# Kernel optimization log

Hardware: AMD Instinct MI355X
Metric: run time of the kernel (lower is better)

Reference implementation:

```python
import jax, jax.numpy as jnp
import numpy as np


def setup_inputs() -> dict:
    key = jax.random.key(0)
    ks = jax.random.split(key, 6)
    SEQ, B, N_INP, N_HID, N_OUT = 2048, 128, 64, 128, 10
    # orthogonal-ish init scales (rand_ortho produces orthogonal matrices; we use
    # scaled gaussians as stand-ins since exact values don't affect the op pattern)
    x = jax.random.normal(ks[0], (SEQ, B, N_INP), dtype=jnp.float32)
    Wxh = jax.random.normal(ks[1], (N_INP, N_HID), dtype=jnp.float32) * np.sqrt(1.0 / N_INP).astype(np.float32)
    Whh = jax.random.normal(ks[2], (N_HID, N_HID), dtype=jnp.float32) * np.sqrt(1.0 / N_HID).astype(np.float32)
    Why = jax.random.normal(ks[3], (N_HID, N_OUT), dtype=jnp.float32) * np.sqrt(1.0 / N_HID).astype(np.float32)
    bh = jnp.zeros((N_HID,), dtype=jnp.float32)
    by = jnp.zeros((N_OUT,), dtype=jnp.float32)
    return {"x": x, "Wxh": Wxh, "Whh": Whh, "Why": Why, "bh": bh, "by": by}


def reference(x, Wxh, Whh, Why, bh, by):
    # x: [seq_len, batch, n_inp]
    seq_len, batch, _ = x.shape
    n_hid = Whh.shape[0]
    # precompute the input projection for all timesteps in one big GEMM
    xW = jnp.einsum('sbi,ih->sbh', x, Wxh) + bh  # [S, B, H]

    def step(h_prev, xw_t):
        h_t = jnp.tanh(h_prev @ Whh + xw_t)
        return h_t, h_t

    h0 = jnp.zeros((batch, n_hid), dtype=x.dtype)
    h_last, h = jax.lax.scan(step, h0, xW)  # h: [S, B, H]
    logits = h_last @ Why + by  # [B, n_out]
    return (logits, h)
```

## Files before the change

### kernel.cpp

```cpp
#include <hip/hip_runtime.h>
#include <math.h>

#define SEQ   2048
#define BATCH  128
#define NINP    64
#define NHID   128
#define NOUT    10
#define CH      64
#define NCHUNK (SEQ / CH)

typedef const float __attribute__((address_space(1)))* gptr_t;
typedef float       __attribute__((address_space(3)))* lptr_t;

__global__ __launch_bounds__(256) void proj_kernel(const float* __restrict__ x,
                                                   const float* __restrict__ Wxh,
                                                   const float* __restrict__ bh,
                                                   float* __restrict__ xw) {
    __shared__ float Wlds[NINP * NHID];
    __shared__ float xs[32 * NINP];
    const int t = threadIdx.x;
    const size_t r0 = (size_t)blockIdx.x * 32;

#pragma unroll
    for (int i = 0; i < 8; ++i)
        ((float4*)Wlds)[t + 256 * i] = ((const float4*)Wxh)[t + 256 * i];
    const float4* xg = (const float4*)(x + r0 * NINP);
    ((float4*)xs)[t]       = xg[t];
    ((float4*)xs)[t + 256] = xg[t + 256];
    __syncthreads();

    const int tj = t & 31;
    const int tr = t >> 5;
    const int j  = 4 * tj;
    const float4 bhv = *(const float4*)(bh + j);
    float acc[4][4];
#pragma unroll
    for (int r = 0; r < 4; ++r) {
        acc[r][0] = bhv.x; acc[r][1] = bhv.y; acc[r][2] = bhv.z; acc[r][3] = bhv.w;
    }
#pragma unroll 8
    for (int i = 0; i < NINP; ++i) {
        const float4 w4 = *(const float4*)&Wlds[i * NHID + j];
#pragma unroll
        for (int r = 0; r < 4; ++r) {
            const float xv = xs[(4 * tr + r) * NINP + i];
            acc[r][0] = fmaf(xv, w4.x, acc[r][0]);
            acc[r][1] = fmaf(xv, w4.y, acc[r][1]);
            acc[r][2] = fmaf(xv, w4.z, acc[r][2]);
            acc[r][3] = fmaf(xv, w4.w, acc[r][3]);
        }
    }
#pragma unroll
    for (int r = 0; r < 4; ++r) {
        float4 o = { acc[r][0], acc[r][1], acc[r][2], acc[r][3] };
        *(float4*)(xw + (r0 + 4 * tr + r) * NHID + j) = o;
    }
}

__global__ __launch_bounds__(256) void scan_kernel(const float* __restrict__ Whh,
                                                   float* __restrict__ hbuf) {
    __shared__ float xwc[2][CH][NHID];
    __shared__ float P[2][4][NHID];

    const int b  = blockIdx.x;
    const int t  = threadIdx.x;
    const int w  = t >> 6;
    const int l  = t & 63;
    const int jj = l & 31;
    const int j0 = 32 * w;

    float wx[32], wy[32];
    {
        const float* wp = Whh + (size_t)j0 * NHID + l;
#pragma unroll
        for (int i = 0; i < 32; ++i) {
            wx[i] = wp[(size_t)i * NHID];
            wy[i] = wp[(size_t)i * NHID + 64];
        }
#pragma unroll
        for (int i = 0; i < 32; ++i) {
            asm volatile("" : "+v"(wx[i]));
            asm volatile("" : "+v"(wy[i]));
        }
    }

    float* rowbase = hbuf + (size_t)b * NHID;

    auto issue_chunk = [&](int c, int nb) {
#pragma unroll
        for (int i = 0; i < 8; ++i) {
            const int f  = (i * 4 + w) * 256 + l * 4;
            const int tl = f >> 7;
            const int jx = f & 127;
            const float* gp = hbuf + ((size_t)(c * CH + tl) * BATCH + b) * NHID + jx;
            lptr_t lp = (lptr_t)&xwc[nb][0][0] + (i * 4 + w) * 256;
            __builtin_amdgcn_global_load_lds((gptr_t)gp, lp, 16, 0, 0);
        }
    };

    issue_chunk(0, 0);
    asm volatile("s_waitcnt vmcnt(0)" ::: "memory");
    __syncthreads();

    float vh = 0.f;
    int cbuf = 0;

    for (int c = 0; c < NCHUNK; ++c) {
        if (c + 1 < NCHUNK) issue_chunk(c + 1, cbuf ^ 1);

#pragma unroll 2
        for (int ts = 0; ts < CH; ++ts) {
            const int pb = ts & 1;
            const float xwv = xwc[cbuf][ts][j0 + jj];

            float ax = 0.f, ay = 0.f;
#pragma unroll
            for (int i = 0; i < 32; ++i) {
                const float hr = __uint_as_float(
                    __builtin_amdgcn_readlane(__float_as_uint(vh), i));
                ax = fmaf(hr, wx[i], ax);
                ay = fmaf(hr, wy[i], ay);
            }
            P[pb][w][l]      = ax;
            P[pb][w][l + 64] = ay;

            asm volatile("s_waitcnt lgkmcnt(0)" ::: "memory");
            __builtin_amdgcn_s_barrier();
            __builtin_amdgcn_sched_barrier(0);

            const float p0 = P[pb][0][j0 + jj];
            const float p1 = P[pb][1][j0 + jj];
            const float p2 = P[pb][2][j0 + jj];
            const float p3 = P[pb][3][j0 + jj];
            const float z  = ((p0 + p1) + (p2 + p3)) + xwv;

            const float zc = fminf(fmaxf(z, -15.f), 15.f);
            const float e  = __builtin_amdgcn_exp2f(zc * 2.8853900817779268f);
            const float hv = (e - 1.f) * __builtin_amdgcn_rcpf(e + 1.f);
            vh = hv;

            if (l < 32)
                rowbase[(size_t)(c * CH + ts) * BATCH * NHID + j0 + l] = hv;
        }

        asm volatile("s_waitcnt vmcnt(0)" ::: "memory");
        __builtin_amdgcn_s_barrier();
        __builtin_amdgcn_sched_barrier(0);
        cbuf ^= 1;
    }
}

__global__ __launch_bounds__(256) void head_kernel(const float* __restrict__ hlast,
                                                   const float* __restrict__ Why,
                                                   const float* __restrict__ by,
                                                   float* __restrict__ out) {
    const int idx = blockIdx.x * 256 + threadIdx.x;
    if (idx >= BATCH * NOUT) return;
    const int b = idx / NOUT;
    const int o = idx % NOUT;
    const float* h = hlast + (size_t)b * NHID;
    float acc = by[o];
#pragma unroll 8
    for (int k = 0; k < NHID; ++k)
        acc = fmaf(h[k], Why[(size_t)k * NOUT + o], acc);
    out[idx] = acc;
}

extern "C" void kernel_launch(void* const* d_in, const int* in_sizes, int n_in,
                              void* d_out, int out_size, void* d_ws, size_t ws_size,
                              hipStream_t stream) {
    const float* x   = (const float*)d_in[0];
    const float* Wxh = (const float*)d_in[1];
    const float* Whh = (const float*)d_in[2];
    const float* Why = (const float*)d_in[3];
    const float* bh  = (const float*)d_in[4];
    const float* by  = (const float*)d_in[5];
    float* out  = (float*)d_out;
    float* hreg = out + BATCH * NOUT;

    proj_kernel<<<(SEQ * BATCH) / 32, 256, 0, stream>>>(x, Wxh, bh, hreg);
    scan_kernel<<<BATCH, 256, 0, stream>>>(Whh, hreg);
    head_kernel<<<5, 256, 0, stream>>>(hreg + (size_t)(SEQ - 1) * BATCH * NHID,
                                       Why, by, out);
}
```

Before: 1.220 ms.

## Process four batch rows per scan block with register prefetch of input projections

The recurrent scan kernel now gives each block four batch rows instead of one and launches 32 blocks instead of 128. The rows' matvecs are interleaved within one timestep so each barrier and LDS round-trip is shared by four independent dependency chains. The LDS double-buffered chunk prefetch of the input projection is replaced by a three-step-ahead register prefetch from global memory. The partial-sum buffer is transposed so the four wave partials are read with one float4 load. The trade-off is about four times more serial FMA and readlane work per step within a block, and most CUs now sit idle.

```diff
diff --git a/kernel.cpp b/kernel.cpp
--- a/kernel.cpp
+++ b/kernel.cpp
@@ -6,11 +6,8 @@
 #define NINP    64
 #define NHID   128
 #define NOUT    10
-#define CH      64
-#define NCHUNK (SEQ / CH)
-
-typedef const float __attribute__((address_space(1)))* gptr_t;
-typedef float       __attribute__((address_space(3)))* lptr_t;
+#define RPB      4
+#define NBLK  (BATCH / RPB)
 
 __global__ __launch_bounds__(256) void proj_kernel(const float* __restrict__ x,
                                                    const float* __restrict__ Wxh,
@@ -59,15 +56,14 @@
 
 __global__ __launch_bounds__(256) void scan_kernel(const float* __restrict__ Whh,
                                                    float* __restrict__ hbuf) {
-    __shared__ float xwc[2][CH][NHID];
-    __shared__ float P[2][4][NHID];
+    __shared__ float P[2][RPB][NHID][4];
 
-    const int b  = blockIdx.x;
     const int t  = threadIdx.x;
     const int w  = t >> 6;
     const int l  = t & 63;
     const int jj = l & 31;
     const int j0 = 32 * w;
+    const int r0 = blockIdx.x * RPB;
 
     float wx[32], wy[32];
     {
@@ -84,69 +80,58 @@
         }
     }
 
-    float* rowbase = hbuf + (size_t)b * NHID;
+    float vh[RPB], xc[RPB], x1[RPB], x2[RPB];
+#pragma unroll
+    for (int r = 0; r < RPB; ++r) {
+        vh[r] = 0.f;
+        const float* p = hbuf + ((size_t)(r0 + r)) * NHID + j0 + jj;
+        xc[r] = p[0];
+        x1[r] = p[(size_t)1 * BATCH * NHID];
+        x2[r] = p[(size_t)2 * BATCH * NHID];
+    }
 
-    auto issue_chunk = [&](int c, int nb) {
+    for (int ts = 0; ts < SEQ; ++ts) {
+        const int pb = ts & 1;
+
 #pragma unroll
-        for (int i = 0; i < 8; ++i) {
-            const int f  = (i * 4 + w) * 256 + l * 4;
-            const int tl = f >> 7;
-            const int jx = f & 127;
-            const float* gp = hbuf + ((size_t)(c * CH + tl) * BATCH + b) * NHID + jx;
-            lptr_t lp = (lptr_t)&xwc[nb][0][0] + (i * 4 + w) * 256;
-            __builtin_amdgcn_global_load_lds((gptr_t)gp, lp, 16, 0, 0);
-        }
-    };
-
-    issue_chunk(0, 0);
-    asm volatile("s_waitcnt vmcnt(0)" ::: "memory");
-    __syncthreads();
-
-    float vh = 0.f;
-    int cbuf = 0;
-
-    for (int c = 0; c < NCHUNK; ++c) {
-        if (c + 1 < NCHUNK) issue_chunk(c + 1, cbuf ^ 1);
-
-#pragma unroll 2
-        for (int ts = 0; ts < CH; ++ts) {
-            const int pb = ts & 1;
-            const float xwv = xwc[cbuf][ts][j0 + jj];
-
+        for (int r = 0; r < RPB; ++r) {
             float ax = 0.f, ay = 0.f;
 #pragma unroll
-            for (int i = 0; i < 32; ++i) {
-                const float hr = __uint_as_float(
-                    __builtin_amdgcn_readlane(__float_as_uint(vh), i));
-                ax = fmaf(hr, wx[i], ax);
-                ay = fmaf(hr, wy[i], ay);
+            for (int g = 0; g < 4; ++g) {
+                float hr[8];
+#pragma unroll
+                for (int i = 0; i < 8; ++i)
+                    hr[i] = __uint_as_float(__builtin_amdgcn_readlane(
+                        __float_as_uint(vh[r]), 8 * g + i));
+#pragma unroll
+                for (int i = 0; i < 8; ++i) {
+                    ax = fmaf(hr[i], wx[8 * g + i], ax);
+                    ay = fmaf(hr[i], wy[8 * g + i], ay);
+                }
             }
-            P[pb][w][l]      = ax;
-            P[pb][w][l + 64] = ay;
+            P[pb][r][l][w]      = ax;
+            P[pb][r][64 + l][w] = ay;
+        }
 
-            asm volatile("s_waitcnt lgkmcnt(0)" ::: "memory");
-            __builtin_amdgcn_s_barrier();
-            __builtin_amdgcn_sched_barrier(0);
+        asm volatile("s_waitcnt lgkmcnt(0)" ::: "memory");
+        __builtin_amdgcn_s_barrier();
+        asm volatile("" ::: "memory");
 
-            const float p0 = P[pb][0][j0 + jj];
-            const float p1 = P[pb][1][j0 + jj];
-            const float p2 = P[pb][2][j0 + jj];
-            const float p3 = P[pb][3][j0 + jj];
-            const float z  = ((p0 + p1) + (p2 + p3)) + xwv;
-
+#pragma unroll
+        for (int r = 0; r < RPB; ++r) {
+            const float4 p4 = *(const float4*)&P[pb][r][j0 + jj][0];
+            const float z  = ((p4.x + p4.y) + (p4.z + p4.w)) + xc[r];
             const float zc = fminf(fmaxf(z, -15.f), 15.f);
             const float e  = __builtin_amdgcn_exp2f(zc * 2.8853900817779268f);
             const float hv = (e - 1.f) * __builtin_amdgcn_rcpf(e + 1.f);
-            vh = hv;
-
-            if (l < 32)
-                rowbase[(size_t)(c * CH + ts) * BATCH * NHID + j0 + l] = hv;
+            vh[r] = hv;
+            hbuf[((size_t)ts * BATCH + (r0 + r)) * NHID + j0 + jj] = hv;
+            xc[r] = x1[r]; x1[r] = x2[r];
         }
-
-        asm volatile("s_waitcnt vmcnt(0)" ::: "memory");
-        __builtin_amdgcn_s_barrier();
-        __builtin_amdgcn_sched_barrier(0);
-        cbuf ^= 1;
+        const int tt = (ts + 3 < SEQ) ? (ts + 3) : (SEQ - 1);
+#pragma unroll
+        for (int r = 0; r < RPB; ++r)
+            x2[r] = hbuf[((size_t)tt * BATCH + (r0 + r)) * NHID + j0 + jj];
     }
 }
 
@@ -179,7 +164,7 @@
     float* hreg = out + BATCH * NOUT;
 
     proj_kernel<<<(SEQ * BATCH) / 32, 256, 0, stream>>>(x, Wxh, bh, hreg);
-    scan_kernel<<<BATCH, 256, 0, stream>>>(Whh, hreg);
+    scan_kernel<<<NBLK, 256, 0, stream>>>(Whh, hreg);
     head_kernel<<<5, 256, 0, stream>>>(hreg + (size_t)(SEQ - 1) * BATCH * NHID,
                                        Why, by, out);
 }
```

Result: slower. 3.019 ms (+147.5%).
